# Kernel tuning notes

Measured on AMD Instinct MI355X. Metric: run time of the kernel, lower is better.

Reference implementation:

```python
import jax, jax.numpy as jnp
import numpy as np

NUM_HEADS = 8


def setup_inputs() -> dict:
    key = jax.random.key(0)
    ks = jax.random.split(key, 7)
    B, C, H, W = 4, 256, 56, 56
    hd = C // NUM_HEADS  # 32
    x = jax.random.normal(ks[0], (B, C, H, W), dtype=jnp.float32)
    # Grouped 1x1 conv (groups=num_heads): per-group (head_dim -> head_dim) linear maps.
    # Stored as (heads, out_per_group, in_per_group), equivalent to torch weight
    # [C, C//groups, 1, 1] reshaped to (heads, hd, hd).
    s = 1.0 / np.sqrt(hd)
    Wq = jax.random.uniform(ks[1], (NUM_HEADS, hd, hd), jnp.float32, -s, s)
    bq = jax.random.uniform(ks[2], (NUM_HEADS, hd), jnp.float32, -s, s)
    Wk = jax.random.uniform(ks[3], (NUM_HEADS, hd, hd), jnp.float32, -s, s)
    bk = jax.random.uniform(ks[4], (NUM_HEADS, hd), jnp.float32, -s, s)
    Wv = jax.random.uniform(ks[5], (NUM_HEADS, hd, hd), jnp.float32, -s, s)
    bv = jax.random.uniform(ks[6], (NUM_HEADS, hd), jnp.float32, -s, s)
    return {"x": x, "Wq": Wq, "bq": bq, "Wk": Wk, "bk": bk, "Wv": Wv, "bv": bv}


def reference(x, Wq, bq, Wk, bk, Wv, bv):
    B, C, H, W = x.shape
    G = NUM_HEADS
    hd = C // G
    L = H * W
    # (B, G, hd, L): grouped channels flattened over space
    xg = x.reshape(B, G, hd, L)
    # grouped 1x1 convs == per-group linear over channel dim
    q = jnp.einsum('goi,bgil->bgol', Wq, xg) + bq[None, :, :, None]
    k = jnp.einsum('goi,bgil->bgol', Wk, xg) + bk[None, :, :, None]
    v = jnp.einsum('goi,bgil->bgol', Wv, xg) + bv[None, :, :, None]
    # energy = q^T k : (B, G, L, L); note: NO 1/sqrt(d) scaling in original
    energy = jnp.einsum('bgdi,bgdj->bgij', q, k)
    attn = jax.nn.softmax(energy, axis=-1)
    # original: out = bmm(value, attention) -> out[d,k] = sum_j V[d,j] * A[j,k]
    out = jnp.einsum('bgdj,bgjk->bgdk', v, attn)
    return out.reshape(B, C, H, W) + x
```

## Files before the change

### kernel.cpp

```cpp
#include <hip/hip_runtime.h>

#define NUM_G 8
#define HD    32
#define LSP   3136
#define BG    32
#define TPB   256
#define LOG2E 1.4426950408889634f

typedef short bf16x8 __attribute__((ext_vector_type(8)));
typedef short short4v __attribute__((ext_vector_type(4)));
typedef float f32x4  __attribute__((ext_vector_type(4)));
typedef unsigned uint2v __attribute__((ext_vector_type(2)));
typedef unsigned uint4v __attribute__((ext_vector_type(4)));

union B8 { bf16x8 h; uint4v u; };
union U8 { bf16x8 h; uint2v u[2]; };
union U4 { short4v h; unsigned u[2]; };

extern "C" __device__ float __ocml_native_exp2_f32(float);
__device__ __forceinline__ float fast_exp2(float x) {
#if __has_builtin(__builtin_amdgcn_exp2f)
    return __builtin_amdgcn_exp2f(x);
#else
    return __ocml_native_exp2_f32(x);
#endif
}

__device__ __forceinline__ unsigned pk_bf16(float a, float b) {
#if __has_builtin(__builtin_amdgcn_cvt_pk_bf16_f32)
    typedef __bf16 bf16x2_t __attribute__((ext_vector_type(2)));
    bf16x2_t r = __builtin_amdgcn_cvt_pk_bf16_f32(a, b);
    unsigned u; __builtin_memcpy(&u, &r, 4); return u;
#else
    unsigned ua = __float_as_uint(a); ua += 0x7FFFu + ((ua >> 16) & 1u);
    unsigned ub = __float_as_uint(b); ub += 0x7FFFu + ((ub >> 16) & 1u);
    return (ua >> 16) | (ub & 0xFFFF0000u);
#endif
}

__device__ __forceinline__ short f2bf(float f) {
    unsigned u = __float_as_uint(f);
    u += 0x7FFFu + ((u >> 16) & 1u);
    return (short)(u >> 16);
}

__device__ __forceinline__ float bf2f(short s) {
    return __uint_as_float(((unsigned)(unsigned short)s) << 16);
}

__global__ __launch_bounds__(TPB, 4) void qkv_mfma(
    const float* __restrict__ x,
    const float* __restrict__ Wq, const float* __restrict__ bq,
    const float* __restrict__ Wk, const float* __restrict__ bk,
    const float* __restrict__ Wv, const float* __restrict__ bv,
    short* __restrict__ qt, short* __restrict__ kt, short* __restrict__ v)
{
    const int bg = blockIdx.y, gh = bg & (NUM_G - 1);
    const int lane = threadIdx.x & 63, w = threadIdx.x >> 6;
    const int m = lane & 15, g = lane >> 4;

    const float* xb = x + (size_t)bg * HD * LSP;
    short* qtb = qt + (size_t)bg * LSP * HD;
    short* ktb = kt + (size_t)bg * LSP * HD;
    short* vb  = v  + (size_t)bg * HD * LSP;

    B8 wqf[2], wkf[2], wvf[2];
    float bqv[2], bkv[2], bvv[2][4];
#pragma unroll
    for (int h = 0; h < 2; ++h) {
        const int o = 16 * h + m;
        const float* wqp = Wq + (size_t)(gh * HD + o) * HD + 8 * g;
        const float* wkp = Wk + (size_t)(gh * HD + o) * HD + 8 * g;
        const float* wvp = Wv + (size_t)(gh * HD + o) * HD + 8 * g;
#pragma unroll
        for (int p = 0; p < 4; ++p) {
            wqf[h].u[p] = pk_bf16(wqp[2*p] * LOG2E, wqp[2*p+1] * LOG2E);
            wkf[h].u[p] = pk_bf16(wkp[2*p],         wkp[2*p+1]);
            wvf[h].u[p] = pk_bf16(wvp[2*p],         wvp[2*p+1]);
        }
        bqv[h] = bq[gh * HD + o] * LOG2E;
        bkv[h] = bk[gh * HD + o];
#pragma unroll
        for (int r = 0; r < 4; ++r)
            bvv[h][r] = bv[gh * HD + 16 * h + 4 * g + r];
    }

    const int lc = blockIdx.x * 64 + 16 * w;
    const int lrow = lc + m;
    const f32x4 zero = {0.f, 0.f, 0.f, 0.f};
    B8 xf;
#pragma unroll
    for (int p = 0; p < 4; ++p) {
        const float a0 = xb[(size_t)(8*g + 2*p)     * LSP + lrow];
        const float a1 = xb[(size_t)(8*g + 2*p + 1) * LSP + lrow];
        xf.u[p] = pk_bf16(a0, a1);
    }
#pragma unroll
    for (int h = 0; h < 2; ++h) {
        f32x4 cq = __builtin_amdgcn_mfma_f32_16x16x32_bf16(xf.h, wqf[h].h, zero, 0, 0, 0);
        f32x4 ck = __builtin_amdgcn_mfma_f32_16x16x32_bf16(xf.h, wkf[h].h, zero, 0, 0, 0);
        f32x4 cv = __builtin_amdgcn_mfma_f32_16x16x32_bf16(wvf[h].h, xf.h, zero, 0, 0, 0);
#pragma unroll
        for (int r = 0; r < 4; ++r) {
            const int lr = lc + 4 * g + r;
            qtb[(size_t)lr * HD + 16 * h + m] = f2bf(cq[r] + bqv[h]);
            ktb[(size_t)lr * HD + 16 * h + m] = f2bf(ck[r] + bkv[h]);
            vb[(size_t)(16 * h + 4 * g + r) * LSP + lc + m] = f2bf(cv[r] + bvv[h][r]);
        }
    }
}

__global__ __launch_bounds__(TPB, 4) void z_mfma(
    const short* __restrict__ qt, const short* __restrict__ kt,
    short* __restrict__ v)
{
    const int bg = blockIdx.y;
    const int jb = blockIdx.x * 32;
    const int t = threadIdx.x;
    const int lane = t & 63, w = t >> 6, m = lane & 15, g = lane >> 4;

    const short* qtb = qt + (size_t)bg * LSP * HD;
    const short* ktb = kt + (size_t)bg * LSP * HD;
    short* vb = v + (size_t)bg * HD * LSP;

    bf16x8 aq[2];
#pragma unroll
    for (int jq = 0; jq < 2; ++jq)
        aq[jq] = *(const bf16x8*)(qtb + (size_t)(jb + 16 * jq + m) * HD + 8 * g);

    f32x4 zacc[2];
    zacc[0] = (f32x4){0.f, 0.f, 0.f, 0.f};
    zacc[1] = (f32x4){0.f, 0.f, 0.f, 0.f};

    const f32x4 zero = {0.f, 0.f, 0.f, 0.f};
    for (int it = 0; it < 49; ++it) {
        const bf16x8 bkc = *(const bf16x8*)(ktb + (size_t)(it * 64 + 16 * w + m) * HD + 8 * g);
#pragma unroll
        for (int jq = 0; jq < 2; ++jq) {
            f32x4 c = __builtin_amdgcn_mfma_f32_16x16x32_bf16(aq[jq], bkc, zero, 0, 0, 0);
#pragma unroll
            for (int r = 0; r < 4; ++r) zacc[jq][r] += fast_exp2(c[r]);
        }
    }

    __shared__ float zl[32];
    if (t < 32) zl[t] = 0.f;
    __syncthreads();
#pragma unroll
    for (int jq = 0; jq < 2; ++jq) {
#pragma unroll
        for (int r = 0; r < 4; ++r) {
            float s = zacc[jq][r];
            s += __shfl_xor(s, 1); s += __shfl_xor(s, 2);
            s += __shfl_xor(s, 4); s += __shfl_xor(s, 8);
            if (m == 0) atomicAdd(&zl[16 * jq + 4 * g + r], s);
        }
    }
    __syncthreads();

    const int d0 = t >> 3;
    const int jl = (t & 7) * 4;
    float rzv[4];
#pragma unroll
    for (int e = 0; e < 4; ++e) rzv[e] = 1.0f / zl[jl + e];
    short* vp = vb + (size_t)d0 * LSP + jb + jl;
    short4v vv = *(short4v*)vp;
    U4 o;
    o.u[0] = pk_bf16(bf2f(vv[0]) * rzv[0], bf2f(vv[1]) * rzv[1]);
    o.u[1] = pk_bf16(bf2f(vv[2]) * rzv[2], bf2f(vv[3]) * rzv[3]);
    *(short4v*)vp = o.h;
}

__global__ __launch_bounds__(TPB, 4) void out_mfma(
    const short* __restrict__ qt, const short* __restrict__ kt,
    const short* __restrict__ v,
    const float* __restrict__ x, float* __restrict__ out)
{
    const int bg = blockIdx.y;
    const int k0 = blockIdx.x * 64;
    const int lane = threadIdx.x & 63, w = threadIdx.x >> 6;
    const int m = lane & 15, g = lane >> 4;

    const short* qtb = qt + (size_t)bg * LSP * HD;
    const short* ktb = kt + (size_t)bg * LSP * HD;
    const short* vb  = v  + (size_t)bg * HD * LSP;

    bf16x8 bk[4];
#pragma unroll
    for (int ks = 0; ks < 4; ++ks)
        bk[ks] = *(const bf16x8*)(ktb + (size_t)(k0 + 16 * ks + m) * HD + 8 * g);

    __shared__ unsigned lds[4096];
    unsigned* pw = lds + w * 1024;
    const int t2 = 2 * m;
    const int cb = m * 32;

    const f32x4 zero = {0.f, 0.f, 0.f, 0.f};
    f32x4 acc[4][2];
#pragma unroll
    for (int ks = 0; ks < 4; ++ks) { acc[ks][0] = zero; acc[ks][1] = zero; }

    for (int jt = w; jt < 49; jt += 4) {
        const int j0 = jt * 64;

        const bf16x8 av0 = *(const bf16x8*)(vb + (size_t)m        * LSP + j0      + 8 * g);
        const bf16x8 av1 = *(const bf16x8*)(vb + (size_t)m        * LSP + j0 + 32 + 8 * g);
        const bf16x8 av2 = *(const bf16x8*)(vb + (size_t)(16 + m) * LSP + j0      + 8 * g);
        const bf16x8 av3 = *(const bf16x8*)(vb + (size_t)(16 + m) * LSP + j0 + 32 + 8 * g);

        bf16x8 aq[4];
#pragma unroll
        for (int jq = 0; jq < 4; ++jq)
            aq[jq] = *(const bf16x8*)(qtb + (size_t)(j0 + 16 * jq + m) * HD + 8 * g);

        const int blo0 = (4 * g)          ^ t2;
        const int blo1 = (4 * g + 2)      ^ t2;
        const int bhi0 = (16 + 4 * g)     ^ t2;
        const int bhi1 = (16 + 4 * g + 2) ^ t2;

#pragma unroll
        for (int kh = 0; kh < 2; ++kh) {
#pragma unroll
            for (int ks2 = 0; ks2 < 2; ++ks2) {
                const int ks = 2 * kh + ks2;
#pragma unroll
                for (int jq = 0; jq < 4; ++jq) {
                    const f32x4 e = __builtin_amdgcn_mfma_f32_16x16x32_bf16(aq[jq], bk[ks], zero, 0, 0, 0);
                    uint2v w0;
                    w0[0] = pk_bf16(fast_exp2(e[0]), fast_exp2(e[1]));
                    w0[1] = pk_bf16(fast_exp2(e[2]), fast_exp2(e[3]));
                    *(uint2v*)(pw + ks2 * 512 + cb + ((8 * jq + 2 * g) ^ t2)) = w0;
                }
            }
#pragma unroll
            for (int ks2 = 0; ks2 < 2; ++ks2) {
                const int ks = 2 * kh + ks2;
                U8 bplo, bphi;
                bplo.u[0] = *(uint2v*)(pw + ks2 * 512 + cb + blo0);
                bplo.u[1] = *(uint2v*)(pw + ks2 * 512 + cb + blo1);
                bphi.u[0] = *(uint2v*)(pw + ks2 * 512 + cb + bhi0);
                bphi.u[1] = *(uint2v*)(pw + ks2 * 512 + cb + bhi1);
                acc[ks][0] = __builtin_amdgcn_mfma_f32_16x16x32_bf16(av0, bplo.h, acc[ks][0], 0, 0, 0);
                acc[ks][0] = __builtin_amdgcn_mfma_f32_16x16x32_bf16(av1, bphi.h, acc[ks][0], 0, 0, 0);
                acc[ks][1] = __builtin_amdgcn_mfma_f32_16x16x32_bf16(av2, bplo.h, acc[ks][1], 0, 0, 0);
                acc[ks][1] = __builtin_amdgcn_mfma_f32_16x16x32_bf16(av3, bphi.h, acc[ks][1], 0, 0, 0);
            }
        }
    }

    const int t = threadIdx.x;
    float* fl = (float*)lds;
    const size_t bgb = (size_t)bg * HD * LSP;
#pragma unroll
    for (int s = 0; s < 2; ++s) {
        __syncthreads();
#pragma unroll
        for (int ks2 = 0; ks2 < 2; ++ks2) {
            const int ks = 2 * s + ks2;
#pragma unroll
            for (int ds = 0; ds < 2; ++ds)
#pragma unroll
                for (int r = 0; r < 4; ++r) {
                    const int d = 16 * ds + 4 * g + r;
                    fl[w * 1024 + d * 32 + 16 * ks2 + m] = acc[ks][ds][r];
                }
        }
        __syncthreads();
        const int d = t >> 3;
        const int kloc = (t & 7) * 4;
        f32x4 sv = *(f32x4*)(fl + d * 32 + kloc);
#pragma unroll
        for (int wi = 1; wi < 4; ++wi) {
            const f32x4 a = *(f32x4*)(fl + wi * 1024 + d * 32 + kloc);
#pragma unroll
            for (int r = 0; r < 4; ++r) sv[r] += a[r];
        }
        const size_t idx = bgb + (size_t)d * LSP + k0 + 32 * s + kloc;
        const f32x4 xv = *(const f32x4*)(x + idx);
#pragma unroll
        for (int r = 0; r < 4; ++r) sv[r] += xv[r];
        *(f32x4*)(out + idx) = sv;
    }
}

extern "C" void kernel_launch(void* const* d_in, const int* in_sizes, int n_in,
                              void* d_out, int out_size, void* d_ws, size_t ws_size,
                              hipStream_t stream) {
    const float* x  = (const float*)d_in[0];
    const float* Wq = (const float*)d_in[1];
    const float* bq = (const float*)d_in[2];
    const float* Wk = (const float*)d_in[3];
    const float* bk = (const float*)d_in[4];
    const float* Wv = (const float*)d_in[5];
    const float* bv = (const float*)d_in[6];
    float* out = (float*)d_out;

    const size_t QSZ = (size_t)BG * HD * LSP;
    short* qt = (short*)d_ws;
    short* kt = qt + QSZ;
    short* v  = kt + QSZ;

    qkv_mfma<<<dim3(49, BG), TPB, 0, stream>>>(x, Wq, bq, Wk, bk, Wv, bv, qt, kt, v);
    z_mfma  <<<dim3(98, BG), TPB, 0, stream>>>(qt, kt, v);
    out_mfma<<<dim3(49, BG), TPB, 0, stream>>>(qt, kt, v, x, out);
}
```

Measured before the change: 204.7 us.

## Use 512-thread blocks for z and out kernels with wider column tiles

The z kernel now covers 64 query columns per block with 8 waves, splitting the key loop between two wave halves. This halves the grid and doubles the reuse of each K fragment. The out kernel also runs 8 waves per block, splitting the 49 j-tiles across 8 waves instead of 4, and reduces the partial accumulators in two stages through a doubled LDS buffer. Per-wave serial work drops, at the cost of more LDS, an extra reduction barrier, and possibly lower occupancy.

```diff
diff --git a/kernel.cpp b/kernel.cpp
--- a/kernel.cpp
+++ b/kernel.cpp
@@ -4,7 +4,6 @@
 #define HD    32
 #define LSP   3136
 #define BG    32
-#define TPB   256
 #define LOG2E 1.4426950408889634f
 
 typedef short bf16x8 __attribute__((ext_vector_type(8)));
@@ -48,7 +47,7 @@
     return __uint_as_float(((unsigned)(unsigned short)s) << 16);
 }
 
-__global__ __launch_bounds__(TPB, 4) void qkv_mfma(
+__global__ __launch_bounds__(256, 4) void qkv_mfma(
     const float* __restrict__ x,
     const float* __restrict__ Wq, const float* __restrict__ bq,
     const float* __restrict__ Wk, const float* __restrict__ bk,
@@ -110,44 +109,45 @@
     }
 }
 
-__global__ __launch_bounds__(TPB, 4) void z_mfma(
+__global__ __launch_bounds__(512, 4) void z_mfma(
     const short* __restrict__ qt, const short* __restrict__ kt,
     short* __restrict__ v)
 {
     const int bg = blockIdx.y;
-    const int jb = blockIdx.x * 32;
+    const int jb = blockIdx.x * 64;
     const int t = threadIdx.x;
     const int lane = t & 63, w = t >> 6, m = lane & 15, g = lane >> 4;
+    const int wq = w & 3, half = w >> 2;
 
     const short* qtb = qt + (size_t)bg * LSP * HD;
     const short* ktb = kt + (size_t)bg * LSP * HD;
     short* vb = v + (size_t)bg * HD * LSP;
 
-    bf16x8 aq[2];
-#pragma unroll
-    for (int jq = 0; jq < 2; ++jq)
+    bf16x8 aq[4];
+#pragma unroll
+    for (int jq = 0; jq < 4; ++jq)
         aq[jq] = *(const bf16x8*)(qtb + (size_t)(jb + 16 * jq + m) * HD + 8 * g);
 
-    f32x4 zacc[2];
-    zacc[0] = (f32x4){0.f, 0.f, 0.f, 0.f};
-    zacc[1] = (f32x4){0.f, 0.f, 0.f, 0.f};
+    f32x4 zacc[4];
+#pragma unroll
+    for (int jq = 0; jq < 4; ++jq) zacc[jq] = (f32x4){0.f, 0.f, 0.f, 0.f};
 
     const f32x4 zero = {0.f, 0.f, 0.f, 0.f};
-    for (int it = 0; it < 49; ++it) {
-        const bf16x8 bkc = *(const bf16x8*)(ktb + (size_t)(it * 64 + 16 * w + m) * HD + 8 * g);
-#pragma unroll
-        for (int jq = 0; jq < 2; ++jq) {
+    for (int it = half; it < 49; it += 2) {
+        const bf16x8 bkc = *(const bf16x8*)(ktb + (size_t)(it * 64 + 16 * wq + m) * HD + 8 * g);
+#pragma unroll
+        for (int jq = 0; jq < 4; ++jq) {
             f32x4 c = __builtin_amdgcn_mfma_f32_16x16x32_bf16(aq[jq], bkc, zero, 0, 0, 0);
 #pragma unroll
             for (int r = 0; r < 4; ++r) zacc[jq][r] += fast_exp2(c[r]);
         }
     }
 
-    __shared__ float zl[32];
-    if (t < 32) zl[t] = 0.f;
-    __syncthreads();
-#pragma unroll
-    for (int jq = 0; jq < 2; ++jq) {
+    __shared__ float zl[64];
+    if (t < 64) zl[t] = 0.f;
+    __syncthreads();
+#pragma unroll
+    for (int jq = 0; jq < 4; ++jq) {
 #pragma unroll
         for (int r = 0; r < 4; ++r) {
             float s = zacc[jq][r];
@@ -158,8 +158,8 @@
     }
     __syncthreads();
 
-    const int d0 = t >> 3;
-    const int jl = (t & 7) * 4;
+    const int d0 = t >> 4;
+    const int jl = (t & 15) * 4;
     float rzv[4];
 #pragma unroll
     for (int e = 0; e < 4; ++e) rzv[e] = 1.0f / zl[jl + e];
@@ -171,7 +171,7 @@
     *(short4v*)vp = o.h;
 }
 
-__global__ __launch_bounds__(TPB, 4) void out_mfma(
+__global__ __launch_bounds__(512, 4) void out_mfma(
     const short* __restrict__ qt, const short* __restrict__ kt,
     const short* __restrict__ v,
     const float* __restrict__ x, float* __restrict__ out)
@@ -190,7 +190,7 @@
     for (int ks = 0; ks < 4; ++ks)
         bk[ks] = *(const bf16x8*)(ktb + (size_t)(k0 + 16 * ks + m) * HD + 8 * g);
 
-    __shared__ unsigned lds[4096];
+    __shared__ unsigned lds[8192];
     unsigned* pw = lds + w * 1024;
     const int t2 = 2 * m;
     const int cb = m * 32;
@@ -200,7 +200,7 @@
 #pragma unroll
     for (int ks = 0; ks < 4; ++ks) { acc[ks][0] = zero; acc[ks][1] = zero; }
 
-    for (int jt = w; jt < 49; jt += 4) {
+    for (int jt = w; jt < 49; jt += 8) {
         const int j0 = jt * 64;
 
         const bf16x8 av0 = *(const bf16x8*)(vb + (size_t)m        * LSP + j0      + 8 * g);
@@ -248,39 +248,51 @@
         }
     }
 
-    const int t = threadIdx.x;
+    __syncthreads();
     float* fl = (float*)lds;
-    const size_t bgb = (size_t)bg * HD * LSP;
-#pragma unroll
-    for (int s = 0; s < 2; ++s) {
-        __syncthreads();
-#pragma unroll
-        for (int ks2 = 0; ks2 < 2; ++ks2) {
-            const int ks = 2 * s + ks2;
+
+    if (w >= 4) {
+        const int rw = w - 4;
+#pragma unroll
+        for (int ks = 0; ks < 4; ++ks)
 #pragma unroll
             for (int ds = 0; ds < 2; ++ds)
 #pragma unroll
                 for (int r = 0; r < 4; ++r) {
                     const int d = 16 * ds + 4 * g + r;
-                    fl[w * 1024 + d * 32 + 16 * ks2 + m] = acc[ks][ds][r];
+                    fl[rw * 2048 + d * 64 + 16 * ks + m] = acc[ks][ds][r];
                 }
-        }
-        __syncthreads();
-        const int d = t >> 3;
-        const int kloc = (t & 7) * 4;
-        f32x4 sv = *(f32x4*)(fl + d * 32 + kloc);
-#pragma unroll
-        for (int wi = 1; wi < 4; ++wi) {
-            const f32x4 a = *(f32x4*)(fl + wi * 1024 + d * 32 + kloc);
-#pragma unroll
-            for (int r = 0; r < 4; ++r) sv[r] += a[r];
-        }
-        const size_t idx = bgb + (size_t)d * LSP + k0 + 32 * s + kloc;
-        const f32x4 xv = *(const f32x4*)(x + idx);
-#pragma unroll
-        for (int r = 0; r < 4; ++r) sv[r] += xv[r];
-        *(f32x4*)(out + idx) = sv;
-    }
+    }
+    __syncthreads();
+    if (w < 4) {
+#pragma unroll
+        for (int ks = 0; ks < 4; ++ks)
+#pragma unroll
+            for (int ds = 0; ds < 2; ++ds)
+#pragma unroll
+                for (int r = 0; r < 4; ++r) {
+                    const int d = 16 * ds + 4 * g + r;
+                    const int a = w * 2048 + d * 64 + 16 * ks + m;
+                    fl[a] = acc[ks][ds][r] + fl[a];
+                }
+    }
+    __syncthreads();
+
+    const int t = threadIdx.x;
+    const int d = t >> 4;
+    const int kloc = (t & 15) * 4;
+    f32x4 sv = *(f32x4*)(fl + d * 64 + kloc);
+#pragma unroll
+    for (int wi = 1; wi < 4; ++wi) {
+        const f32x4 a = *(f32x4*)(fl + wi * 2048 + d * 64 + kloc);
+#pragma unroll
+        for (int r = 0; r < 4; ++r) sv[r] += a[r];
+    }
+    const size_t idx = (size_t)bg * HD * LSP + (size_t)d * LSP + k0 + kloc;
+    const f32x4 xv = *(const f32x4*)(x + idx);
+#pragma unroll
+    for (int r = 0; r < 4; ++r) sv[r] += xv[r];
+    *(f32x4*)(out + idx) = sv;
 }
 
 extern "C" void kernel_launch(void* const* d_in, const int* in_sizes, int n_in,
@@ -300,7 +312,7 @@
     short* kt = qt + QSZ;
     short* v  = kt + QSZ;
 
-    qkv_mfma<<<dim3(49, BG), TPB, 0, stream>>>(x, Wq, bq, Wk, bk, Wv, bv, qt, kt, v);
-    z_mfma  <<<dim3(98, BG), TPB, 0, stream>>>(qt, kt, v);
-    out_mfma<<<dim3(49, BG), TPB, 0, stream>>>(qt, kt, v, x, out);
-}
+    qkv_mfma<<<dim3(49, BG), 256, 0, stream>>>(x, Wq, bq, Wk, bk, Wv, bv, qt, kt, v);
+    z_mfma  <<<dim3(49, BG), 512, 0, stream>>>(qt, kt, v);
+    out_mfma<<<dim3(49, BG), 512, 0, stream>>>(qt, kt, v, x, out);
+}
```

Result: no change. 204.9 us (+0.1%).
